# Kernel tuning notes

Hardware: AMD Instinct MI355X
Metric: run time of the kernel (lower is better)

The kernel has to match this reference:

```python
import jax, jax.numpy as jnp
import numpy as np

B = 8192
T = 1000
STATE_DIM = 3
HIDDEN = 256
DT = 0.01


def setup_inputs() -> dict:
    key = jax.random.key(0)
    ks = jax.random.split(key, 7)
    initial_state = jax.random.normal(ks[0], (B, STATE_DIM), dtype=jnp.float32)
    t_grid = (jnp.arange(T, dtype=jnp.float32) * DT)
    s = 0.1  # small init scale keeps the ODE well-behaved over the grid
    W1 = jax.random.normal(ks[1], (STATE_DIM, HIDDEN), dtype=jnp.float32) * s
    b1 = jnp.zeros((HIDDEN,), dtype=jnp.float32)
    W2 = jax.random.normal(ks[2], (HIDDEN, HIDDEN), dtype=jnp.float32) * s
    b2 = jnp.zeros((HIDDEN,), dtype=jnp.float32)
    W3 = jax.random.normal(ks[3], (HIDDEN, STATE_DIM), dtype=jnp.float32) * s
    b3 = jnp.zeros((STATE_DIM,), dtype=jnp.float32)
    return {"initial_state": initial_state, "t_grid": t_grid,
            "W1": W1, "b1": b1, "W2": W2, "b2": b2, "W3": W3, "b3": b3}


def reference(initial_state, t_grid, W1, b1, W2, b2, W3, b3):
    # VectorFieldNet: state -> tanh MLP -> dstate/dt (autonomous; ignores t)
    def vf(s):  # s: [B, D]
        h = jnp.tanh(s @ W1 + b1)
        h = jnp.tanh(h @ W2 + b2)
        return h @ W3 + b3

    dts = t_grid[1:] - t_grid[:-1]  # [T-1]

    def step(cur, dt):
        k1 = vf(cur)
        k2 = vf(cur + 0.5 * dt * k1)
        k3 = vf(cur + 0.5 * dt * k2)
        k4 = vf(cur + dt * k3)
        nxt = cur + (dt / 6.0) * (k1 + 2.0 * k2 + 2.0 * k3 + k4)
        return nxt, nxt

    _, traj = jax.lax.scan(step, initial_state, dts)  # [T-1, B, D]
    rollout = jnp.concatenate([initial_state[None], traj], axis=0)  # [T, B, D]
    return jnp.transpose(rollout, (1, 0, 2))  # [B, T, D]
```

## Files before the change

kernel.cpp:

```cpp
#include <hip/hip_runtime.h>

typedef __attribute__((ext_vector_type(8))) short bf16x8;
typedef __attribute__((ext_vector_type(4))) float f32x4;

union FU { unsigned int u[4]; uint4 q; bf16x8 v; };

__device__ inline unsigned int cvt_pk(float lo, float hi) {
    unsigned int r;
    asm("v_cvt_pk_bf16_f32 %0, %1, %2" : "=v"(r) : "v"(lo), "v"(hi));
    return r;
}

__device__ inline float tanh_fast(float x) {
    float e = __expf(x + x);
    return fmaf(-2.f, __builtin_amdgcn_rcpf(e + 1.f), 1.f);
}

#define TS 1000
#define NEV ((TS - 1) * 4)

__global__ __launch_bounds__(512, 4)
void node_ode_kernel(const float* __restrict__ Ig, const float* __restrict__ tg,
                     const float* __restrict__ W1g, const float* __restrict__ b1g,
                     const float* __restrict__ W2g, const float* __restrict__ b2g,
                     const float* __restrict__ W3g, const float* __restrict__ b3g,
                     float* __restrict__ outp)
{
    __shared__ uint4 h1s[16 * 32];
    __shared__ float w3s[256 * 3];
    __shared__ __align__(16) float part2[16][28];

    const int tid  = threadIdx.x;
    const int lane = tid & 63;
    const int wv   = tid >> 6;
    const int nb   = lane & 15;
    const int g4   = lane >> 4;
    const int xm   = nb & 7;
    const int bb0  = blockIdx.x * 16;

    for (int i = tid; i < 768; i += 512) w3s[i] = W3g[i];

    const float b30 = b3g[0], b31 = b3g[1], b32 = b3g[2];
    float4 b2r0 = *(const float4*)&b2g[wv * 32 + g4 * 4];
    float4 b2r1 = *(const float4*)&b2g[wv * 32 + 16 + g4 * 4];

    float y00 = Ig[(bb0 + nb) * 3 + 0];
    float y01 = Ig[(bb0 + nb) * 3 + 1];
    float y02 = Ig[(bb0 + nb) * 3 + 2];
    float yc0 = y00, yc1 = y01, yc2 = y02;
    float ks0 = 0.f, ks1 = 0.f, ks2 = 0.f;
    if (tid < 16) {
        size_t o = (size_t)(bb0 + tid) * (TS * 3);
        outp[o + 0] = y00; outp[o + 1] = y01; outp[o + 2] = y02;
    }

    bf16x8 w2f[2][8];
    {
        const int ncb = wv * 32 + nb;
        #pragma unroll
        for (int mt = 0; mt < 2; ++mt) {
            #pragma unroll
            for (int ks = 0; ks < 8; ++ks) {
                FU f;
                #pragma unroll
                for (int jj = 0; jj < 4; ++jj) {
                    int k0 = ks * 32 + g4 * 8 + jj * 2;
                    f.u[jj] = cvt_pk(W2g[(size_t)k0 * 256 + ncb + mt * 16],
                                     W2g[(size_t)(k0 + 1) * 256 + ncb + mt * 16]);
                }
                w2f[mt][ks] = f.v;
            }
        }
    }

    bf16x8 w1a[2];
    {
        #pragma unroll
        for (int mt = 0; mt < 2; ++mt) {
            const int col = (wv * 2 + mt) * 16 + nb;
            float w0 = W1g[col], w1 = W1g[256 + col], w2 = W1g[512 + col];
            float bb = b1g[col];
            FU f;
            if (g4 == 0) {
                f.u[0] = cvt_pk(w0, w1);
                f.u[1] = cvt_pk(w2, w0);
                f.u[2] = cvt_pk(w1, w2);
                f.u[3] = cvt_pk(bb, 0.f);
            } else if (g4 == 1) {
                unsigned int p01 = cvt_pk(w0, w1);
                unsigned int p2x = cvt_pk(w2, 0.f);
                float w0l = w0 - __uint_as_float(p01 << 16);
                float w1l = w1 - __uint_as_float(p01 & 0xFFFF0000u);
                float w2l = w2 - __uint_as_float(p2x << 16);
                f.u[0] = cvt_pk(w0l, w1l);
                f.u[1] = cvt_pk(w2l, 0.f);
                f.u[2] = 0u; f.u[3] = 0u;
            } else {
                f.u[0] = f.u[1] = f.u[2] = f.u[3] = 0u;
            }
            w1a[mt] = f.v;
        }
    }
    __syncthreads();

    float dtv = tg[1] - tg[0];

    for (int ev = 0; ev < NEV; ++ev) {
        if (ev > 0) {
            float k0, k1, k2;
            {
                float4 a = *(const float4*)&part2[nb][0];
                float4 b = *(const float4*)&part2[nb][4];
                k0 = (((a.x + a.y) + (a.z + a.w)) + ((b.x + b.y) + (b.z + b.w))) + b30;
                a = *(const float4*)&part2[nb][8];
                b = *(const float4*)&part2[nb][12];
                k1 = (((a.x + a.y) + (a.z + a.w)) + ((b.x + b.y) + (b.z + b.w))) + b31;
                a = *(const float4*)&part2[nb][16];
                b = *(const float4*)&part2[nb][20];
                k2 = (((a.x + a.y) + (a.z + a.w)) + ((b.x + b.y) + (b.z + b.w))) + b32;
            }
            const int pph = (ev - 1) & 3;
            if (pph == 0) {
                ks0 = k0; ks1 = k1; ks2 = k2;
                float h = 0.5f * dtv;
                yc0 = fmaf(h, k0, y00); yc1 = fmaf(h, k1, y01); yc2 = fmaf(h, k2, y02);
            } else if (pph == 1) {
                ks0 += 2.f * k0; ks1 += 2.f * k1; ks2 += 2.f * k2;
                float h = 0.5f * dtv;
                yc0 = fmaf(h, k0, y00); yc1 = fmaf(h, k1, y01); yc2 = fmaf(h, k2, y02);
            } else if (pph == 2) {
                ks0 += 2.f * k0; ks1 += 2.f * k1; ks2 += 2.f * k2;
                yc0 = fmaf(dtv, k0, y00); yc1 = fmaf(dtv, k1, y01); yc2 = fmaf(dtv, k2, y02);
            } else {
                float s = dtv * (1.f / 6.f);
                y00 = fmaf(s, ks0 + k0, y00);
                y01 = fmaf(s, ks1 + k1, y01);
                y02 = fmaf(s, ks2 + k2, y02);
                yc0 = y00; yc1 = y01; yc2 = y02;
                const int t = ev >> 2;
                if (tid < 16) {
                    size_t o = (size_t)(bb0 + nb) * (TS * 3) + (size_t)t * 3;
                    outp[o + 0] = y00; outp[o + 1] = y01; outp[o + 2] = y02;
                }
                dtv = tg[t + 1] - tg[t];
            }
        }

        {
            unsigned int u01  = cvt_pk(yc0, yc1);
            float yl0 = yc0 - __uint_as_float(u01 << 16);
            float yl1 = yc1 - __uint_as_float(u01 & 0xFFFF0000u);
            unsigned int u2l0 = cvt_pk(yc2, yl0);
            float yl2 = yc2 - __uint_as_float(u2l0 << 16);
            unsigned int ull  = cvt_pk(yl1, yl2);
            FU bf;
            if (g4 == 0) {
                bf.u[0] = u01; bf.u[1] = u2l0; bf.u[2] = ull; bf.u[3] = 0x00003f80u;
            } else if (g4 == 1) {
                bf.u[0] = u01; bf.u[1] = u2l0 & 0x0000FFFFu; bf.u[2] = 0u; bf.u[3] = 0u;
            } else {
                bf.u[0] = bf.u[1] = bf.u[2] = bf.u[3] = 0u;
            }
            #pragma unroll
            for (int mt = 0; mt < 2; ++mt) {
                f32x4 d = {0.f, 0.f, 0.f, 0.f};
                d = __builtin_amdgcn_mfma_f32_16x16x32_bf16(w1a[mt], bf.v, d, 0, 0, 0);
                float h0 = tanh_fast(d[0]);
                float h1 = tanh_fast(d[1]);
                float h2 = tanh_fast(d[2]);
                float h3 = tanh_fast(d[3]);
                uint2 wq;
                wq.x = cvt_pk(h0, h1);
                wq.y = cvt_pk(h2, h3);
                const int o = (wv * 2 + mt) * 2 + (g4 >> 1);
                *(uint2*)((char*)h1s + nb * 512 + ((o ^ xm) * 16) + ((g4 & 1) * 8)) = wq;
            }
        }
        __syncthreads();

        {
            f32x4 acc0, acc1;
            acc0[0] = b2r0.x; acc0[1] = b2r0.y; acc0[2] = b2r0.z; acc0[3] = b2r0.w;
            acc1[0] = b2r1.x; acc1[1] = b2r1.y; acc1[2] = b2r1.z; acc1[3] = b2r1.w;
            #pragma unroll
            for (int ks = 0; ks < 8; ++ks) {
                FU tm; tm.q = h1s[nb * 32 + ((ks * 4 + g4) ^ xm)];
                acc0 = __builtin_amdgcn_mfma_f32_16x16x32_bf16(w2f[0][ks], tm.v, acc0, 0, 0, 0);
                acc1 = __builtin_amdgcn_mfma_f32_16x16x32_bf16(w2f[1][ks], tm.v, acc1, 0, 0, 0);
            }
            float p0 = 0.f, p1 = 0.f, p2 = 0.f;
            {
                const int row0 = wv * 32 + g4 * 4;
                float4 wa = *(const float4*)&w3s[row0 * 3];
                float4 wb = *(const float4*)&w3s[row0 * 3 + 4];
                float4 wc = *(const float4*)&w3s[row0 * 3 + 8];
                float h;
                h = tanh_fast(acc0[0]); p0 = fmaf(h, wa.x, p0); p1 = fmaf(h, wa.y, p1); p2 = fmaf(h, wa.z, p2);
                h = tanh_fast(acc0[1]); p0 = fmaf(h, wa.w, p0); p1 = fmaf(h, wb.x, p1); p2 = fmaf(h, wb.y, p2);
                h = tanh_fast(acc0[2]); p0 = fmaf(h, wb.z, p0); p1 = fmaf(h, wb.w, p1); p2 = fmaf(h, wc.x, p2);
                h = tanh_fast(acc0[3]); p0 = fmaf(h, wc.y, p0); p1 = fmaf(h, wc.z, p1); p2 = fmaf(h, wc.w, p2);
            }
            {
                const int row0 = wv * 32 + 16 + g4 * 4;
                float4 wa = *(const float4*)&w3s[row0 * 3];
                float4 wb = *(const float4*)&w3s[row0 * 3 + 4];
                float4 wc = *(const float4*)&w3s[row0 * 3 + 8];
                float h;
                h = tanh_fast(acc1[0]); p0 = fmaf(h, wa.x, p0); p1 = fmaf(h, wa.y, p1); p2 = fmaf(h, wa.z, p2);
                h = tanh_fast(acc1[1]); p0 = fmaf(h, wa.w, p0); p1 = fmaf(h, wb.x, p1); p2 = fmaf(h, wb.y, p2);
                h = tanh_fast(acc1[2]); p0 = fmaf(h, wb.z, p0); p1 = fmaf(h, wb.w, p1); p2 = fmaf(h, wc.x, p2);
                h = tanh_fast(acc1[3]); p0 = fmaf(h, wc.y, p0); p1 = fmaf(h, wc.z, p1); p2 = fmaf(h, wc.w, p2);
            }
            p0 += __shfl_xor(p0, 16); p1 += __shfl_xor(p1, 16); p2 += __shfl_xor(p2, 16);
            p0 += __shfl_xor(p0, 32); p1 += __shfl_xor(p1, 32); p2 += __shfl_xor(p2, 32);
            if (lane < 16) {
                part2[lane][wv]      = p0;
                part2[lane][8 + wv]  = p1;
                part2[lane][16 + wv] = p2;
            }
        }
        __syncthreads();
    }

    {
        float4 a = *(const float4*)&part2[nb][0];
        float4 b = *(const float4*)&part2[nb][4];
        float k0 = (((a.x + a.y) + (a.z + a.w)) + ((b.x + b.y) + (b.z + b.w))) + b30;
        a = *(const float4*)&part2[nb][8];
        b = *(const float4*)&part2[nb][12];
        float k1 = (((a.x + a.y) + (a.z + a.w)) + ((b.x + b.y) + (b.z + b.w))) + b31;
        a = *(const float4*)&part2[nb][16];
        b = *(const float4*)&part2[nb][20];
        float k2 = (((a.x + a.y) + (a.z + a.w)) + ((b.x + b.y) + (b.z + b.w))) + b32;
        float s = dtv * (1.f / 6.f);
        y00 = fmaf(s, ks0 + k0, y00);
        y01 = fmaf(s, ks1 + k1, y01);
        y02 = fmaf(s, ks2 + k2, y02);
        if (tid < 16) {
            size_t o = (size_t)(bb0 + nb) * (TS * 3) + (size_t)(TS - 1) * 3;
            outp[o + 0] = y00; outp[o + 1] = y01; outp[o + 2] = y02;
        }
    }
}

extern "C" void kernel_launch(void* const* d_in, const int* in_sizes, int n_in,
                              void* d_out, int out_size, void* d_ws, size_t ws_size,
                              hipStream_t stream) {
    (void)in_sizes; (void)n_in; (void)d_ws; (void)ws_size; (void)out_size;
    const float* Ig  = (const float*)d_in[0];
    const float* tg  = (const float*)d_in[1];
    const float* W1g = (const float*)d_in[2];
    const float* b1g = (const float*)d_in[3];
    const float* W2g = (const float*)d_in[4];
    const float* b2g = (const float*)d_in[5];
    const float* W3g = (const float*)d_in[6];
    const float* b3g = (const float*)d_in[7];
    float* outp = (float*)d_out;

    dim3 grid(512), block(512);
    hipLaunchKernelGGL(node_ode_kernel, grid, block, 0, stream,
                       Ig, tg, W1g, b1g, W2g, b2g, W3g, b3g, outp);
}
```

Measured before the change: 8.159 ms.

## Reduce stage-2 partials via LDS atomics with double-buffered k, padded h1 layout

Replaces the per-wave partial-sum array and its 24-value readback with LDS atomicAdd into a double-buffered k buffer, zeroing the stale buffer each step. Replaces the XOR swizzle of the hidden-activation buffer with a padded row stride, and precomputes dt values into shared memory instead of loading from global memory inside the loop. The aim is to cut LDS reads, address math and global loads on the serial per-step critical path. In exchange, LDS float atomics make the summation order nondeterministic and may serialize, and the padded layout may change bank conflicts.

```diff
diff --git a/kernel.cpp b/kernel.cpp
--- a/kernel.cpp
+++ b/kernel.cpp
@@ -18,6 +18,7 @@
 
 #define TS 1000
 #define NEV ((TS - 1) * 4)
+#define ROWB 528
 
 __global__ __launch_bounds__(512, 4)
 void node_ode_kernel(const float* __restrict__ Ig, const float* __restrict__ tg,
@@ -26,19 +27,24 @@
                      const float* __restrict__ W3g, const float* __restrict__ b3g,
                      float* __restrict__ outp)
 {
-    __shared__ uint4 h1s[16 * 32];
+    __shared__ __align__(16) char h1s[16 * ROWB];
     __shared__ float w3s[256 * 3];
-    __shared__ __align__(16) float part2[16][28];
+    __shared__ float dtss[TS - 1];
+    __shared__ __align__(16) float kbuf[2][16][4];
 
     const int tid  = threadIdx.x;
     const int lane = tid & 63;
     const int wv   = tid >> 6;
     const int nb   = lane & 15;
     const int g4   = lane >> 4;
-    const int xm   = nb & 7;
     const int bb0  = blockIdx.x * 16;
 
+    char* const wr = h1s + nb * ROWB + wv * 64 + g4 * 8;
+    char* const rd = h1s + nb * ROWB + g4 * 16;
+
     for (int i = tid; i < 768; i += 512) w3s[i] = W3g[i];
+    for (int i = tid; i < TS - 1; i += 512) dtss[i] = tg[i + 1] - tg[i];
+    if (tid < 128) ((float*)kbuf)[tid] = 0.f;
 
     const float b30 = b3g[0], b31 = b3g[1], b32 = b3g[2];
     float4 b2r0 = *(const float4*)&b2g[wv * 32 + g4 * 4];
@@ -103,36 +109,25 @@
     }
     __syncthreads();
 
-    float dtv = tg[1] - tg[0];
-
     for (int ev = 0; ev < NEV; ++ev) {
         if (ev > 0) {
-            float k0, k1, k2;
-            {
-                float4 a = *(const float4*)&part2[nb][0];
-                float4 b = *(const float4*)&part2[nb][4];
-                k0 = (((a.x + a.y) + (a.z + a.w)) + ((b.x + b.y) + (b.z + b.w))) + b30;
-                a = *(const float4*)&part2[nb][8];
-                b = *(const float4*)&part2[nb][12];
-                k1 = (((a.x + a.y) + (a.z + a.w)) + ((b.x + b.y) + (b.z + b.w))) + b31;
-                a = *(const float4*)&part2[nb][16];
-                b = *(const float4*)&part2[nb][20];
-                k2 = (((a.x + a.y) + (a.z + a.w)) + ((b.x + b.y) + (b.z + b.w))) + b32;
-            }
+            float4 kv = *(const float4*)&kbuf[ev & 1][nb][0];
+            float k0 = kv.x + b30, k1 = kv.y + b31, k2 = kv.z + b32;
+            float dtc = dtss[(ev - 1) >> 2];
             const int pph = (ev - 1) & 3;
             if (pph == 0) {
                 ks0 = k0; ks1 = k1; ks2 = k2;
-                float h = 0.5f * dtv;
+                float h = 0.5f * dtc;
                 yc0 = fmaf(h, k0, y00); yc1 = fmaf(h, k1, y01); yc2 = fmaf(h, k2, y02);
             } else if (pph == 1) {
                 ks0 += 2.f * k0; ks1 += 2.f * k1; ks2 += 2.f * k2;
-                float h = 0.5f * dtv;
+                float h = 0.5f * dtc;
                 yc0 = fmaf(h, k0, y00); yc1 = fmaf(h, k1, y01); yc2 = fmaf(h, k2, y02);
             } else if (pph == 2) {
                 ks0 += 2.f * k0; ks1 += 2.f * k1; ks2 += 2.f * k2;
-                yc0 = fmaf(dtv, k0, y00); yc1 = fmaf(dtv, k1, y01); yc2 = fmaf(dtv, k2, y02);
+                yc0 = fmaf(dtc, k0, y00); yc1 = fmaf(dtc, k1, y01); yc2 = fmaf(dtc, k2, y02);
             } else {
-                float s = dtv * (1.f / 6.f);
+                float s = dtc * (1.f / 6.f);
                 y00 = fmaf(s, ks0 + k0, y00);
                 y01 = fmaf(s, ks1 + k1, y01);
                 y02 = fmaf(s, ks2 + k2, y02);
@@ -142,7 +137,6 @@
                     size_t o = (size_t)(bb0 + nb) * (TS * 3) + (size_t)t * 3;
                     outp[o + 0] = y00; outp[o + 1] = y01; outp[o + 2] = y02;
                 }
-                dtv = tg[t + 1] - tg[t];
             }
         }
 
@@ -165,15 +159,10 @@
             for (int mt = 0; mt < 2; ++mt) {
                 f32x4 d = {0.f, 0.f, 0.f, 0.f};
                 d = __builtin_amdgcn_mfma_f32_16x16x32_bf16(w1a[mt], bf.v, d, 0, 0, 0);
-                float h0 = tanh_fast(d[0]);
-                float h1 = tanh_fast(d[1]);
-                float h2 = tanh_fast(d[2]);
-                float h3 = tanh_fast(d[3]);
                 uint2 wq;
-                wq.x = cvt_pk(h0, h1);
-                wq.y = cvt_pk(h2, h3);
-                const int o = (wv * 2 + mt) * 2 + (g4 >> 1);
-                *(uint2*)((char*)h1s + nb * 512 + ((o ^ xm) * 16) + ((g4 & 1) * 8)) = wq;
+                wq.x = cvt_pk(tanh_fast(d[0]), tanh_fast(d[1]));
+                wq.y = cvt_pk(tanh_fast(d[2]), tanh_fast(d[3]));
+                *(uint2*)(wr + mt * 32) = wq;
             }
         }
         __syncthreads();
@@ -184,7 +173,7 @@
             acc1[0] = b2r1.x; acc1[1] = b2r1.y; acc1[2] = b2r1.z; acc1[3] = b2r1.w;
             #pragma unroll
             for (int ks = 0; ks < 8; ++ks) {
-                FU tm; tm.q = h1s[nb * 32 + ((ks * 4 + g4) ^ xm)];
+                FU tm; tm.q = *(const uint4*)(rd + ks * 64);
                 acc0 = __builtin_amdgcn_mfma_f32_16x16x32_bf16(w2f[0][ks], tm.v, acc0, 0, 0, 0);
                 acc1 = __builtin_amdgcn_mfma_f32_16x16x32_bf16(w2f[1][ks], tm.v, acc1, 0, 0, 0);
             }
@@ -213,26 +202,22 @@
             }
             p0 += __shfl_xor(p0, 16); p1 += __shfl_xor(p1, 16); p2 += __shfl_xor(p2, 16);
             p0 += __shfl_xor(p0, 32); p1 += __shfl_xor(p1, 32); p2 += __shfl_xor(p2, 32);
+            float* kw = &kbuf[(ev + 1) & 1][0][0];
             if (lane < 16) {
-                part2[lane][wv]      = p0;
-                part2[lane][8 + wv]  = p1;
-                part2[lane][16 + wv] = p2;
-            }
+                atomicAdd(&kw[nb * 4 + 0], p0);
+                atomicAdd(&kw[nb * 4 + 1], p1);
+                atomicAdd(&kw[nb * 4 + 2], p2);
+            }
+            if (wv == 7) ((float*)&kbuf[ev & 1][0][0])[lane] = 0.f;
         }
         __syncthreads();
     }
 
     {
-        float4 a = *(const float4*)&part2[nb][0];
-        float4 b = *(const float4*)&part2[nb][4];
-        float k0 = (((a.x + a.y) + (a.z + a.w)) + ((b.x + b.y) + (b.z + b.w))) + b30;
-        a = *(const float4*)&part2[nb][8];
-        b = *(const float4*)&part2[nb][12];
-        float k1 = (((a.x + a.y) + (a.z + a.w)) + ((b.x + b.y) + (b.z + b.w))) + b31;
-        a = *(const float4*)&part2[nb][16];
-        b = *(const float4*)&part2[nb][20];
-        float k2 = (((a.x + a.y) + (a.z + a.w)) + ((b.x + b.y) + (b.z + b.w))) + b32;
-        float s = dtv * (1.f / 6.f);
+        float4 kv = *(const float4*)&kbuf[NEV & 1][nb][0];
+        float k0 = kv.x + b30, k1 = kv.y + b31, k2 = kv.z + b32;
+        float dtc = dtss[(NEV - 1) >> 2];
+        float s = dtc * (1.f / 6.f);
         y00 = fmaf(s, ks0 + k0, y00);
         y01 = fmaf(s, ks1 + k1, y01);
         y02 = fmaf(s, ks2 + k2, y02);
```

Result: slower. 11.20 ms (+37.3%).
